# Optimization experiments

Hardware: AMD Instinct MI355X
Metric: run time of the kernel (lower is better)

Reference implementation:

```python
import jax, jax.numpy as jnp
import numpy as np

B = 1
DIM = 2048
N_HEADS = 16
HEAD_DIM = 128
RANK = 128
ALPHA = 128.0
L_NOISE = 2048
L_COND = 1024
N_LORAS = 1
EPS = 1e-6
NEG = -1e20


def setup_inputs() -> dict:
    key = jax.random.key(0)
    ks = jax.random.split(key, 24)
    inp = {}
    inp["noise_flat"] = jax.random.normal(ks[0], (B, L_NOISE, DIM), jnp.float32)
    inp["cond_flat"] = jax.random.normal(ks[1], (B, L_COND, DIM), jnp.float32)
    # RoPE freqs in TE 'bshd' convention: (L, head_dim), halves duplicated
    inv_freq = 1.0 / (10000.0 ** (jnp.arange(0, HEAD_DIM, 2, dtype=jnp.float32) / HEAD_DIM))
    pos = jnp.arange(L_NOISE + L_COND, dtype=jnp.float32)
    fr = pos[:, None] * inv_freq[None, :]
    fr = jnp.concatenate([fr, fr], axis=-1)  # (L, HEAD_DIM)
    inp["noise_rope"] = fr[:L_NOISE]
    inp["cond_rope"] = fr[L_NOISE:]
    std = 0.02
    inp["Wq"] = jax.random.normal(ks[2], (DIM, DIM), jnp.float32) * std
    inp["Wk"] = jax.random.normal(ks[3], (DIM, DIM), jnp.float32) * std
    inp["Wv"] = jax.random.normal(ks[4], (DIM, DIM), jnp.float32) * std
    inp["Wo"] = jax.random.normal(ks[5], (DIM, DIM), jnp.float32) * std
    inp["bq"] = jnp.zeros((DIM,), jnp.float32)
    inp["bk"] = jnp.zeros((DIM,), jnp.float32)
    inp["bv"] = jnp.zeros((DIM,), jnp.float32)
    inp["bo"] = jnp.zeros((DIM,), jnp.float32)
    inp["q_norm_scale"] = jnp.ones((HEAD_DIM,), jnp.float32)
    inp["k_norm_scale"] = jnp.ones((HEAD_DIM,), jnp.float32)
    inp["v_norm_scale"] = jnp.ones((HEAD_DIM,), jnp.float32)
    # LoRA: down ~ N(0, 1/rank); up small nonzero (torch inits zeros, made nonzero for a meaningful baseline)
    for name, ki in zip(["q", "k", "v", "o"], range(6, 10)):
        k1, k2 = jax.random.split(ks[ki])
        inp[f"lora_{name}_down"] = jax.random.normal(k1, (DIM, RANK), jnp.float32) / RANK
        inp[f"lora_{name}_up"] = jax.random.normal(k2, (RANK, DIM), jnp.float32) * 0.01
    return inp


def _rms_norm(x, scale):
    return x * jax.lax.rsqrt(jnp.mean(x * x, axis=-1, keepdims=True) + EPS) * scale


def _rotate_half(x):
    x1, x2 = jnp.split(x, 2, axis=-1)
    return jnp.concatenate([-x2, x1], axis=-1)


def _apply_rope(x, freqs):
    # x: (B, L, H, D), freqs: (L, D)
    cos = jnp.cos(freqs)[None, :, None, :]
    sin = jnp.sin(freqs)[None, :, None, :]
    return x * cos + _rotate_half(x) * sin


def _block_mask():
    # noise rows attend to everything; cond block i attends only to itself
    L = L_NOISE + L_COND * N_LORAS
    idx = jnp.arange(L)
    is_noise = idx < L_NOISE
    blk = (idx - L_NOISE) // L_COND
    allowed = is_noise[:, None] | (
        (~is_noise[:, None]) & (~is_noise[None, :]) & (blk[:, None] == blk[None, :])
    )
    return jnp.where(allowed, 0.0, NEG).astype(jnp.float32)  # (L, L)


def _cond_mask(i, L):
    idx = jnp.arange(L)
    start = L_NOISE + i * L_COND
    return ((idx >= start) & (idx < start + L_COND)).astype(jnp.float32)[None, :, None]


def reference(noise_flat, cond_flat, noise_rope, cond_rope,
              Wq, Wk, Wv, Wo, bq, bk, bv, bo,
              q_norm_scale, k_norm_scale, v_norm_scale,
              lora_q_down, lora_q_up, lora_k_down, lora_k_up,
              lora_v_down, lora_v_up, lora_o_down, lora_o_up):
    joint = jnp.concatenate([noise_flat, cond_flat], axis=1)  # (B, L, D)
    rope = jnp.concatenate([noise_rope, cond_rope], axis=0)   # (L, HEAD_DIM)
    L = joint.shape[1]
    scale_lora = ALPHA / RANK
    m = _cond_mask(0, L)  # n_loras = 1, lora_weight = 1.0
    jm = joint * m

    def lora(x_masked, Wd, Wu):
        return (x_masked @ Wd) @ Wu * scale_lora

    q = joint @ Wq + bq + lora(jm, lora_q_down, lora_q_up)
    k = joint @ Wk + bk + lora(jm, lora_k_down, lora_k_up)
    v = joint @ Wv + bv + lora(jm, lora_v_down, lora_v_up)

    q = q.reshape(B, L, N_HEADS, HEAD_DIM)
    k = k.reshape(B, L, N_HEADS, HEAD_DIM)
    v = v.reshape(B, L, N_HEADS, HEAD_DIM)
    q = _rms_norm(q, q_norm_scale)
    k = _rms_norm(k, k_norm_scale)
    v = _rms_norm(v, v_norm_scale)
    q = _apply_rope(q, rope)
    k = _apply_rope(k, rope)

    bias = _block_mask()[None, None]  # (1,1,L,L)
    scores = jnp.einsum('bqhd,bkhd->bhqk', q, k) / jnp.sqrt(jnp.float32(HEAD_DIM)) + bias
    attn = jax.nn.softmax(scores, axis=-1)
    x = jnp.einsum('bhqk,bkhd->bqhd', attn, v).reshape(B, L, DIM)

    out = x @ Wo + bo + lora(x * m, lora_o_down, lora_o_up)
    return out[:, :L_NOISE, :], out[:, L_NOISE:, :]
```

## Files before the change

kernel.cpp:

```cpp
#include <hip/hip_runtime.h>

typedef _Float16 f16;
typedef _Float16 half8 __attribute__((ext_vector_type(8)));
typedef float floatx4 __attribute__((ext_vector_type(4)));

#define L_TOT   3072
#define L_NZ    2048
#define DIM_C   2048
#define NH      16
#define HD      128

__device__ __forceinline__ void gl_lds16(const f16* g, f16* l) {
    __builtin_amdgcn_global_load_lds((__attribute__((address_space(1))) void*)g,
                                     (__attribute__((address_space(3))) void*)l,
                                     16, 0, 0);
}

__global__ void sentinel_kernel(float* out) { out[0] = 1.0e6f; }

__global__ __launch_bounds__(256)
void cast_f32_f16(const float* __restrict__ in, f16* __restrict__ out, int n) {
    int i = (blockIdx.x * 256 + threadIdx.x) * 4;
    if (i + 3 < n) {
        float4 v = *(const float4*)(in + i);
        out[i+0] = (f16)v.x; out[i+1] = (f16)v.y;
        out[i+2] = (f16)v.z; out[i+3] = (f16)v.w;
    }
}

template<typename TIN>
__global__ __launch_bounds__(256)
void transpose_cast(const TIN* __restrict__ in, f16* __restrict__ out,
                    int R, int C, long long inBatch, long long outBatch) {
    in  += (long long)blockIdx.z * inBatch;
    out += (long long)blockIdx.z * outBatch;
    __shared__ f16 tile[32][33];
    int x = threadIdx.x & 31, y0 = threadIdx.x >> 5;
    int r0 = blockIdx.y * 32, c0 = blockIdx.x * 32;
#pragma unroll
    for (int i = 0; i < 4; ++i) {
        int y = y0 + i * 8;
        tile[y][x] = (f16)(float)in[(size_t)(r0 + y) * C + (c0 + x)];
    }
    __syncthreads();
#pragma unroll
    for (int i = 0; i < 4; ++i) {
        int y = y0 + i * 8;
        out[(size_t)(c0 + y) * R + (r0 + x)] = tile[x][y];
    }
}

template<int WRITE_HALF, int ACCUM, int ADD_BIAS, int SPLIT3>
__global__ __launch_bounds__(256, 2)
void gemm_tn(const f16* __restrict__ A, const f16* __restrict__ BT,
             void* __restrict__ Cv,
             const float* __restrict__ bias0, const float* __restrict__ bias1,
             const float* __restrict__ bias2,
             int M, int N, int K, int lda, int ldb, int ldc, float cscale) {
    __shared__ __align__(16) f16 lds[2][2][128 * 64];
    const int tid  = threadIdx.x;
    const int lane = tid & 63, wave = tid >> 6;
    const int m0 = blockIdx.y * 128, n0 = blockIdx.x * 128;
    const int wr = wave >> 1, wc = wave & 1;
    floatx4 acc[4][4] = {};

    const int r0i = tid >> 3;
    const int gch = (tid & 7) ^ (r0i & 7);
    const f16* gA0 = A  + (size_t)(m0 + r0i) * lda + gch * 8;
    const f16* gB0 = BT + (size_t)(n0 + r0i) * ldb + gch * 8;
    const int ldsW = wave * 512;

    auto stage = [&](int buf, int k0) {
#pragma unroll
        for (int is = 0; is < 4; ++is)
            gl_lds16(gA0 + k0 + (size_t)is * 32 * lda, &lds[buf][0][0] + is * 2048 + ldsW);
#pragma unroll
        for (int is = 0; is < 4; ++is)
            gl_lds16(gB0 + k0 + (size_t)is * 32 * ldb, &lds[buf][1][0] + is * 2048 + ldsW);
    };

    const int rl = lane & 15, cq = lane >> 4;

    const int nIter = K >> 6;
    stage(0, 0);
    int cur = 0;
    for (int t = 0; t < nIter; ++t) {
        const int k0n = (t + 1 < nIter) ? (t + 1) * 64 : 0;
        stage(cur ^ 1, k0n);
        asm volatile("s_waitcnt vmcnt(8)" ::: "memory");
        __builtin_amdgcn_s_barrier();
        __builtin_amdgcn_sched_barrier(0);

#pragma unroll
        for (int kh = 0; kh < 2; ++kh) {
            half8 af[4], bf[4];
#pragma unroll
            for (int m = 0; m < 4; ++m) {
                int row = wr * 64 + m * 16 + rl;
                int pos = (kh * 4 + cq) ^ (row & 7);
                af[m] = *(const half8*)(&lds[cur][0][row * 64 + pos * 8]);
            }
#pragma unroll
            for (int n = 0; n < 4; ++n) {
                int row = wc * 64 + n * 16 + rl;
                int pos = (kh * 4 + cq) ^ (row & 7);
                bf[n] = *(const half8*)(&lds[cur][1][row * 64 + pos * 8]);
            }
#pragma unroll
            for (int m = 0; m < 4; ++m)
#pragma unroll
                for (int n = 0; n < 4; ++n)
                    acc[m][n] = __builtin_amdgcn_mfma_f32_16x16x32_f16(af[m], bf[n], acc[m][n], 0, 0, 0);
        }
        __builtin_amdgcn_s_barrier();
        __builtin_amdgcn_sched_barrier(0);
        cur ^= 1;
    }

    const int rq = lane >> 4;
    const float* bias = bias0;
    size_t cbase = 0;
    if (SPLIT3) {
        int chunk = n0 >> 11;
        bias = (chunk == 0) ? bias0 : ((chunk == 1) ? bias1 : bias2);
        cbase = (size_t)chunk * ((size_t)L_TOT * DIM_C);
    }
#pragma unroll
    for (int m = 0; m < 4; ++m) {
        int row = m0 + wr * 64 + m * 16 + rq * 4;
#pragma unroll
        for (int n = 0; n < 4; ++n) {
            int col = n0 + wc * 64 + n * 16 + rl;
            float badd = ADD_BIAS ? bias[SPLIT3 ? (col & 2047) : col] : 0.0f;
            int ccol = SPLIT3 ? (col & 2047) : col;
#pragma unroll
            for (int j = 0; j < 4; ++j) {
                float v = acc[m][n][j] * cscale + badd;
                size_t idx = cbase + (size_t)(row + j) * ldc + ccol;
                if (WRITE_HALF) {
                    f16* C = (f16*)Cv;
                    if (ACCUM) v += (float)C[idx];
                    C[idx] = (f16)v;
                } else {
                    float* C = (float*)Cv;
                    if (ACCUM) v += C[idx];
                    C[idx] = v;
                }
            }
        }
    }
}

__global__ __launch_bounds__(128)
void norm_rope_kernel(const f16* __restrict__ q16, const f16* __restrict__ k16, const f16* __restrict__ v16,
                      const float* __restrict__ qs, const float* __restrict__ ks, const float* __restrict__ vs,
                      const float* __restrict__ nrope, const float* __restrict__ crope,
                      f16* __restrict__ qH, f16* __restrict__ kH, f16* __restrict__ vH) {
    const int r = blockIdx.x, h = blockIdx.y, d = threadIdx.x;
    const size_t src = (size_t)r * DIM_C + h * HD + d;
    float qv = (float)q16[src], kv = (float)k16[src], vv = (float)v16[src];
    float sq = qv * qv, sk = kv * kv, sv = vv * vv;
#pragma unroll
    for (int m = 1; m < 64; m <<= 1) {
        sq += __shfl_xor(sq, m);
        sk += __shfl_xor(sk, m);
        sv += __shfl_xor(sv, m);
    }
    __shared__ float part[3][2];
    const int wid = d >> 6;
    if ((d & 63) == 0) { part[0][wid] = sq; part[1][wid] = sk; part[2][wid] = sv; }
    __syncthreads();
    float rq = rsqrtf((part[0][0] + part[0][1]) * (1.0f / 128.0f) + 1e-6f);
    float rk = rsqrtf((part[1][0] + part[1][1]) * (1.0f / 128.0f) + 1e-6f);
    float rv = rsqrtf((part[2][0] + part[2][1]) * (1.0f / 128.0f) + 1e-6f);
    float qn = qv * rq * qs[d];
    float kn = kv * rk * ks[d];
    float vn = vv * rv * vs[d];
    __shared__ float shq[128], shk[128];
    shq[d] = qn; shk[d] = kn;
    __syncthreads();
    float rotq = (d < 64) ? -shq[d + 64] : shq[d - 64];
    float rotk = (d < 64) ? -shk[d + 64] : shk[d - 64];
    const float* rp = (r < L_NZ) ? (nrope + (size_t)r * HD) : (crope + (size_t)(r - L_NZ) * HD);
    float fr = rp[d];
    float c = cosf(fr), s = sinf(fr);
    const size_t dst = ((size_t)h * L_TOT + r) * HD + d;
    qH[dst] = (f16)((qn * c + rotq * s) * 0.08838834764831845f);
    kH[dst] = (f16)(kn * c + rotk * s);
    vH[dst] = (f16)vn;
}

__global__ __launch_bounds__(256, 2)
void flash_kernel(const f16* __restrict__ qH, const f16* __restrict__ kH,
                  const f16* __restrict__ vT, f16* __restrict__ xH) {
    __shared__ __align__(16) f16 lds_k[2][64 * 128];
    __shared__ __align__(16) f16 lds_v[64 * 128];
    __shared__ __align__(16) f16 p_lds[4][32][72];
    const int tid = threadIdx.x;
    const int lane = tid & 63, w = tid >> 6;
    const int bid = blockIdx.x;
    const int xcd = bid & 7, rr = bid >> 3;
    int h, qb;
    if (rr < 16) { h = xcd + 8 * (rr >> 3); qb = 16 + (rr & 7); }
    else         { int li = rr - 16; h = xcd + 8 * (li >> 4); qb = li & 15; }
    const int q0 = qb * 128 + w * 32;
    const int rl = lane & 15, rq = lane >> 4;

    half8 aq[2][4];
    const f16* qbase = qH + ((size_t)h * L_TOT + q0) * HD;
#pragma unroll
    for (int qt = 0; qt < 2; ++qt)
#pragma unroll
        for (int kc = 0; kc < 4; ++kc)
            aq[qt][kc] = *(const half8*)(qbase + (size_t)(qt * 16 + rl) * HD + kc * 32 + rq * 8);

    floatx4 acc[2][8] = {};
    floatx4 accl[2] = {};
    const half8 vone = {(f16)1.f, (f16)1.f, (f16)1.f, (f16)1.f,
                        (f16)1.f, (f16)1.f, (f16)1.f, (f16)1.f};

    const int kLo = (qb >= 16) ? L_NZ : 0;
    const f16* khead = kH + (size_t)h * L_TOT * HD;
    const f16* vhead = vT + (size_t)h * HD * L_TOT;

    auto stageK = [&](int kb, int pb) {
#pragma unroll
        for (int is = 0; is < 4; ++is) {
            int i = is * 256 + tid;
            int r = i >> 4, c = i & 15;
            gl_lds16(khead + (size_t)(kb + r) * HD + ((c ^ (r & 15)) * 8),
                     &lds_k[pb][0] + (is * 256 + w * 64) * 8);
        }
    };
    auto stageV = [&](int kb) {
#pragma unroll
        for (int is = 0; is < 4; ++is) {
            int i = is * 256 + tid;
            int pair = i >> 4, c10 = i & 15;
            int g10 = c10 ^ (pair & 15);
            int d = pair * 2 + (g10 >> 3), kchunk = g10 & 7;
            gl_lds16(vhead + (size_t)d * L_TOT + kb + kchunk * 8,
                     lds_v + (is * 256 + w * 64) * 8);
        }
    };

    asm volatile("s_waitcnt vmcnt(0)" ::: "memory");
    stageK(kLo, 0);
    int p = 0;
    for (int kb = kLo; kb < L_TOT; kb += 64) {
        const int kbn = (kb + 64 < L_TOT) ? (kb + 64) : kLo;
        stageV(kb);
        stageK(kbn, p ^ 1);
        asm volatile("s_waitcnt vmcnt(8)" ::: "memory");
        __builtin_amdgcn_s_barrier();
        __builtin_amdgcn_sched_barrier(0);

        const f16* kbase = &lds_k[p][0];
        floatx4 sacc[2][4] = {};
#pragma unroll
        for (int kf = 0; kf < 4; ++kf) {
            int r = kf * 16 + rl;
#pragma unroll
            for (int kc = 0; kc < 4; ++kc) {
                half8 bk = *(const half8*)(kbase + r * 128 + (((kc * 4 + rq) ^ (r & 15)) * 8));
                sacc[0][kf] = __builtin_amdgcn_mfma_f32_16x16x32_f16(aq[0][kc], bk, sacc[0][kf], 0, 0, 0);
                sacc[1][kf] = __builtin_amdgcn_mfma_f32_16x16x32_f16(aq[1][kc], bk, sacc[1][kf], 0, 0, 0);
            }
        }
#pragma unroll
        for (int qt = 0; qt < 2; ++qt)
#pragma unroll
            for (int kf = 0; kf < 4; ++kf)
#pragma unroll
                for (int j = 0; j < 4; ++j) {
                    float pv = __expf(sacc[qt][kf][j] - 4.0f);
                    p_lds[w][qt * 16 + rq * 4 + j][kf * 16 + rl] = (f16)pv;
                }

        asm volatile("s_waitcnt vmcnt(4)" ::: "memory");
        __builtin_amdgcn_s_barrier();
        __builtin_amdgcn_sched_barrier(0);

#pragma unroll
        for (int kc = 0; kc < 2; ++kc) {
            half8 ap0 = *(const half8*)(&p_lds[w][0 * 16 + rl][kc * 32 + rq * 8]);
            half8 ap1 = *(const half8*)(&p_lds[w][1 * 16 + rl][kc * 32 + rq * 8]);
            accl[0] = __builtin_amdgcn_mfma_f32_16x16x32_f16(ap0, vone, accl[0], 0, 0, 0);
            accl[1] = __builtin_amdgcn_mfma_f32_16x16x32_f16(ap1, vone, accl[1], 0, 0, 0);
#pragma unroll
            for (int dt = 0; dt < 8; ++dt) {
                int d = dt * 16 + rl;
                int g10 = (d & 1) * 8 + kc * 4 + rq;
                half8 bv = *(const half8*)(lds_v + (d >> 1) * 128 + ((g10 ^ ((d >> 1) & 15)) * 8));
                acc[0][dt] = __builtin_amdgcn_mfma_f32_16x16x32_f16(ap0, bv, acc[0][dt], 0, 0, 0);
                acc[1][dt] = __builtin_amdgcn_mfma_f32_16x16x32_f16(ap1, bv, acc[1][dt], 0, 0, 0);
            }
        }
        __builtin_amdgcn_s_barrier();
        p ^= 1;
    }

#pragma unroll
    for (int qt = 0; qt < 2; ++qt)
#pragma unroll
        for (int j = 0; j < 4; ++j) {
            float li = 1.0f / accl[qt][j];
            int row = q0 + qt * 16 + rq * 4 + j;
#pragma unroll
            for (int dt = 0; dt < 8; ++dt)
                xH[(size_t)row * DIM_C + h * HD + dt * 16 + rl] = (f16)(acc[qt][dt][j] * li);
        }
}

extern "C" void kernel_launch(void* const* d_in, const int* in_sizes, int n_in,
                              void* d_out, int out_size, void* d_ws, size_t ws_size,
                              hipStream_t stream) {
    const float* noise = (const float*)d_in[0];
    const float* cond  = (const float*)d_in[1];
    const float* nrope = (const float*)d_in[2];
    const float* crope = (const float*)d_in[3];
    const float* Wq = (const float*)d_in[4];
    const float* Wk = (const float*)d_in[5];
    const float* Wv = (const float*)d_in[6];
    const float* Wo = (const float*)d_in[7];
    const float* bq = (const float*)d_in[8];
    const float* bk = (const float*)d_in[9];
    const float* bv = (const float*)d_in[10];
    const float* bo = (const float*)d_in[11];
    const float* qs = (const float*)d_in[12];
    const float* ks = (const float*)d_in[13];
    const float* vs = (const float*)d_in[14];
    const float* lqd = (const float*)d_in[15];
    const float* lqu = (const float*)d_in[16];
    const float* lkd = (const float*)d_in[17];
    const float* lku = (const float*)d_in[18];
    const float* lvd = (const float*)d_in[19];
    const float* lvu = (const float*)d_in[20];
    const float* lod = (const float*)d_in[21];
    const float* lou = (const float*)d_in[22];
    (void)in_sizes; (void)n_in; (void)out_size;

    char* ws = (char*)d_ws;
    const size_t SZ_LD = (size_t)L_TOT * DIM_C * sizeof(f16);
    const size_t SZ_W  = (size_t)DIM_C * DIM_C * sizeof(f16);
    size_t o = 0;
    auto take = [&](size_t b) { size_t r = o; o += (b + 255) & ~(size_t)255; return r; };
    f16* jointH   = (f16*)(ws + take(SZ_LD));
    f16* WTqkv    = (f16*)(ws + take(3 * SZ_W));
    f16* WT3      = (f16*)(ws + take(SZ_W));
    f16* downTqkv = (f16*)(ws + take((size_t)384 * 2048 * 2));
    f16* downTo   = (f16*)(ws + take((size_t)128 * 2048 * 2));
    f16* upT0     = (f16*)(ws + take((size_t)2048 * 128 * 2));
    f16* upT1     = (f16*)(ws + take((size_t)2048 * 128 * 2));
    f16* upT2     = (f16*)(ws + take((size_t)2048 * 128 * 2));
    f16* upTo     = (f16*)(ws + take((size_t)2048 * 128 * 2));
    f16* q16      = (f16*)(ws + take(3 * SZ_LD));
    f16* k16      = q16 + (size_t)L_TOT * DIM_C;
    f16* v16      = k16 + (size_t)L_TOT * DIM_C;
    f16* t_all    = (f16*)(ws + take((size_t)1024 * 384 * 2));
    f16* t_o      = (f16*)(ws + take((size_t)1024 * 128 * 2));
    f16* qHd      = (f16*)(ws + take(SZ_LD));
    f16* kHd      = (f16*)(ws + take(SZ_LD));
    f16* vHd      = (f16*)(ws + take(SZ_LD));
    f16* vTd      = (f16*)(ws + take(SZ_LD));
    f16* xH       = (f16*)(ws + take(SZ_LD));
    if (o > ws_size) {
        sentinel_kernel<<<1, 1, 0, stream>>>((float*)d_out);
        return;
    }

    cast_f32_f16<<<dim3((2048 * 2048) / 1024), 256, 0, stream>>>(noise, jointH, 2048 * 2048);
    cast_f32_f16<<<dim3((1024 * 2048) / 1024), 256, 0, stream>>>(cond, jointH + (size_t)2048 * 2048, 1024 * 2048);
    transpose_cast<float><<<dim3(64, 64, 1), 256, 0, stream>>>(Wq, WTqkv,                          2048, 2048, 0, 0);
    transpose_cast<float><<<dim3(64, 64, 1), 256, 0, stream>>>(Wk, WTqkv + (size_t)2048 * 2048,     2048, 2048, 0, 0);
    transpose_cast<float><<<dim3(64, 64, 1), 256, 0, stream>>>(Wv, WTqkv + (size_t)2 * 2048 * 2048, 2048, 2048, 0, 0);
    transpose_cast<float><<<dim3(64, 64, 1), 256, 0, stream>>>(Wo, WT3, 2048, 2048, 0, 0);
    transpose_cast<float><<<dim3(4, 64, 1), 256, 0, stream>>>(lqd, downTqkv,                      2048, 128, 0, 0);
    transpose_cast<float><<<dim3(4, 64, 1), 256, 0, stream>>>(lkd, downTqkv + (size_t)128 * 2048, 2048, 128, 0, 0);
    transpose_cast<float><<<dim3(4, 64, 1), 256, 0, stream>>>(lvd, downTqkv + (size_t)256 * 2048, 2048, 128, 0, 0);
    transpose_cast<float><<<dim3(4, 64, 1), 256, 0, stream>>>(lod, downTo, 2048, 128, 0, 0);
    transpose_cast<float><<<dim3(64, 4, 1), 256, 0, stream>>>(lqu, upT0, 128, 2048, 0, 0);
    transpose_cast<float><<<dim3(64, 4, 1), 256, 0, stream>>>(lku, upT1, 128, 2048, 0, 0);
    transpose_cast<float><<<dim3(64, 4, 1), 256, 0, stream>>>(lvu, upT2, 128, 2048, 0, 0);
    transpose_cast<float><<<dim3(64, 4, 1), 256, 0, stream>>>(lou, upTo, 128, 2048, 0, 0);

    gemm_tn<1, 0, 1, 1><<<dim3(6144 / 128, 3072 / 128), 256, 0, stream>>>(
        jointH, WTqkv, q16, bq, bk, bv, 3072, 6144, 2048, 2048, 2048, 2048, 1.0f);
    gemm_tn<1, 0, 0, 0><<<dim3(3, 8), 256, 0, stream>>>(jointH + (size_t)2048 * 2048, downTqkv, t_all,
                                                        nullptr, nullptr, nullptr,
                                                        1024, 384, 2048, 2048, 2048, 384, 1.0f);
    dim3 gup(2048 / 128, 1024 / 128);
    gemm_tn<1, 1, 0, 0><<<gup, 256, 0, stream>>>(t_all + 0,   upT0, q16 + (size_t)2048 * 2048,
                                                 nullptr, nullptr, nullptr, 1024, 2048, 128, 384, 128, 2048, 1.0f);
    gemm_tn<1, 1, 0, 0><<<gup, 256, 0, stream>>>(t_all + 128, upT1, k16 + (size_t)2048 * 2048,
                                                 nullptr, nullptr, nullptr, 1024, 2048, 128, 384, 128, 2048, 1.0f);
    gemm_tn<1, 1, 0, 0><<<gup, 256, 0, stream>>>(t_all + 256, upT2, v16 + (size_t)2048 * 2048,
                                                 nullptr, nullptr, nullptr, 1024, 2048, 128, 384, 128, 2048, 1.0f);

    norm_rope_kernel<<<dim3(3072, 16), 128, 0, stream>>>(q16, k16, v16, qs, ks, vs, nrope, crope, qHd, kHd, vHd);
    transpose_cast<f16><<<dim3(4, 96, 16), 256, 0, stream>>>(vHd, vTd, 3072, 128,
                                                             (long long)3072 * 128, (long long)128 * 3072);

    flash_kernel<<<dim3(384), 256, 0, stream>>>(qHd, kHd, vTd, xH);

    gemm_tn<0, 0, 1, 0><<<dim3(16, 24), 256, 0, stream>>>(xH, WT3, d_out, bo, nullptr, nullptr,
                                                          3072, 2048, 2048, 2048, 2048, 2048, 1.0f);
    gemm_tn<1, 0, 0, 0><<<dim3(1, 8), 256, 0, stream>>>(xH + (size_t)2048 * 2048, downTo, t_o,
                                                        nullptr, nullptr, nullptr,
                                                        1024, 128, 2048, 2048, 2048, 128, 1.0f);
    gemm_tn<0, 1, 0, 0><<<gup, 256, 0, stream>>>(t_o, upTo, (float*)d_out + (size_t)2048 * 2048,
                                                 nullptr, nullptr, nullptr,
                                                 1024, 2048, 128, 128, 128, 2048, 1.0f);
}
```

Measured before the change: 402.6 us.

## Batch preprocessing launches, merge LoRA-up GEMMs, fuse V transpose into norm-rope

Merges the two input casts into one launch, the twelve weight transposes into three z-batched launches, and the three LoRA up-projection GEMMs into a single launch whose A pointer is offset per output chunk. The norm/RoPE kernel is rewritten to process 32 rows per block with vectorized half8 loads and stores, and it writes V already transposed through an LDS tile, removing a separate transpose kernel and an intermediate buffer. The flash kernel also raises wave priority around its MFMA sections. Together these cut launch count and memory traffic, at the cost of a more complex norm kernel with heavier register use.

After: 355.6 us. -11.7%, faster.

```diff
diff --git a/kernel.cpp b/kernel.cpp
--- a/kernel.cpp
+++ b/kernel.cpp
@@ -19,28 +19,30 @@
 __global__ void sentinel_kernel(float* out) { out[0] = 1.0e6f; }
 
 __global__ __launch_bounds__(256)
-void cast_f32_f16(const float* __restrict__ in, f16* __restrict__ out, int n) {
+void cast_joint(const float* __restrict__ noise, const float* __restrict__ cond,
+                f16* __restrict__ out) {
     int i = (blockIdx.x * 256 + threadIdx.x) * 4;
-    if (i + 3 < n) {
-        float4 v = *(const float4*)(in + i);
-        out[i+0] = (f16)v.x; out[i+1] = (f16)v.y;
-        out[i+2] = (f16)v.z; out[i+3] = (f16)v.w;
-    }
-}
-
-template<typename TIN>
+    const float* src; int off;
+    if (i < 2048 * 2048) { src = noise; off = i; }
+    else                 { src = cond;  off = i - 2048 * 2048; }
+    float4 v = *(const float4*)(src + off);
+    out[i+0] = (f16)v.x; out[i+1] = (f16)v.y;
+    out[i+2] = (f16)v.z; out[i+3] = (f16)v.w;
+}
+
 __global__ __launch_bounds__(256)
-void transpose_cast(const TIN* __restrict__ in, f16* __restrict__ out,
-                    int R, int C, long long inBatch, long long outBatch) {
-    in  += (long long)blockIdx.z * inBatch;
-    out += (long long)blockIdx.z * outBatch;
+void transpose_cast4(const float* __restrict__ s0, const float* __restrict__ s1,
+                     const float* __restrict__ s2, const float* __restrict__ s3,
+                     f16* __restrict__ dstBase, int R, int C, long long outBatch) {
+    const float* in = (blockIdx.z == 0) ? s0 : (blockIdx.z == 1) ? s1 : (blockIdx.z == 2) ? s2 : s3;
+    f16* out = dstBase + (long long)blockIdx.z * outBatch;
     __shared__ f16 tile[32][33];
     int x = threadIdx.x & 31, y0 = threadIdx.x >> 5;
     int r0 = blockIdx.y * 32, c0 = blockIdx.x * 32;
 #pragma unroll
     for (int i = 0; i < 4; ++i) {
         int y = y0 + i * 8;
-        tile[y][x] = (f16)(float)in[(size_t)(r0 + y) * C + (c0 + x)];
+        tile[y][x] = (f16)in[(size_t)(r0 + y) * C + (c0 + x)];
     }
     __syncthreads();
 #pragma unroll
@@ -50,7 +52,7 @@
     }
 }
 
-template<int WRITE_HALF, int ACCUM, int ADD_BIAS, int SPLIT3>
+template<int WRITE_HALF, int ACCUM, int ADD_BIAS, int MODE>
 __global__ __launch_bounds__(256, 2)
 void gemm_tn(const f16* __restrict__ A, const f16* __restrict__ BT,
              void* __restrict__ Cv,
@@ -64,6 +66,8 @@
     const int wr = wave >> 1, wc = wave & 1;
     floatx4 acc[4][4] = {};
 
+    if (MODE == 2) A += (size_t)(n0 >> 11) * 128;
+
     const int r0i = tid >> 3;
     const int gch = (tid & 7) ^ (r0i & 7);
     const f16* gA0 = A  + (size_t)(m0 + r0i) * lda + gch * 8;
@@ -120,9 +124,9 @@
     const int rq = lane >> 4;
     const float* bias = bias0;
     size_t cbase = 0;
-    if (SPLIT3) {
+    if (MODE == 1 || MODE == 2) {
         int chunk = n0 >> 11;
-        bias = (chunk == 0) ? bias0 : ((chunk == 1) ? bias1 : bias2);
+        if (MODE == 1) bias = (chunk == 0) ? bias0 : ((chunk == 1) ? bias1 : bias2);
         cbase = (size_t)chunk * ((size_t)L_TOT * DIM_C);
     }
 #pragma unroll
@@ -131,8 +135,8 @@
 #pragma unroll
         for (int n = 0; n < 4; ++n) {
             int col = n0 + wc * 64 + n * 16 + rl;
-            float badd = ADD_BIAS ? bias[SPLIT3 ? (col & 2047) : col] : 0.0f;
-            int ccol = SPLIT3 ? (col & 2047) : col;
+            int ccol = (MODE == 1 || MODE == 2) ? (col & 2047) : col;
+            float badd = ADD_BIAS ? bias[ccol] : 0.0f;
 #pragma unroll
             for (int j = 0; j < 4; ++j) {
                 float v = acc[m][n][j] * cscale + badd;
@@ -151,43 +155,65 @@
     }
 }
 
-__global__ __launch_bounds__(128)
-void norm_rope_kernel(const f16* __restrict__ q16, const f16* __restrict__ k16, const f16* __restrict__ v16,
-                      const float* __restrict__ qs, const float* __restrict__ ks, const float* __restrict__ vs,
-                      const float* __restrict__ nrope, const float* __restrict__ crope,
-                      f16* __restrict__ qH, f16* __restrict__ kH, f16* __restrict__ vH) {
-    const int r = blockIdx.x, h = blockIdx.y, d = threadIdx.x;
-    const size_t src = (size_t)r * DIM_C + h * HD + d;
-    float qv = (float)q16[src], kv = (float)k16[src], vv = (float)v16[src];
-    float sq = qv * qv, sk = kv * kv, sv = vv * vv;
-#pragma unroll
-    for (int m = 1; m < 64; m <<= 1) {
-        sq += __shfl_xor(sq, m);
-        sk += __shfl_xor(sk, m);
-        sv += __shfl_xor(sv, m);
-    }
-    __shared__ float part[3][2];
-    const int wid = d >> 6;
-    if ((d & 63) == 0) { part[0][wid] = sq; part[1][wid] = sk; part[2][wid] = sv; }
+__global__ __launch_bounds__(256)
+void norm_rope_v(const f16* __restrict__ q16, const f16* __restrict__ k16, const f16* __restrict__ v16,
+                 const float* __restrict__ qs, const float* __restrict__ ks, const float* __restrict__ vs,
+                 const float* __restrict__ nrope, const float* __restrict__ crope,
+                 f16* __restrict__ qH, f16* __restrict__ kH, f16* __restrict__ vT) {
+    __shared__ f16 vtile[128][33];
+    const int t = threadIdx.x, rloc = t >> 3, c = t & 7;
+    const int r = blockIdx.x * 32 + rloc, h = blockIdx.y;
+    const int d0 = c * 8;
+    const size_t src = (size_t)r * DIM_C + h * HD;
+    half8 qlv = *(const half8*)(q16 + src + d0);
+    half8 qhv = *(const half8*)(q16 + src + 64 + d0);
+    half8 klv = *(const half8*)(k16 + src + d0);
+    half8 khv = *(const half8*)(k16 + src + 64 + d0);
+    half8 vlv = *(const half8*)(v16 + src + d0);
+    half8 vhv = *(const half8*)(v16 + src + 64 + d0);
+    float ql[8], qh[8], kl[8], kh[8], vl[8], vh[8];
+    float sq = 0.f, sk = 0.f, sv = 0.f;
+#pragma unroll
+    for (int i = 0; i < 8; ++i) {
+        ql[i] = (float)qlv[i]; qh[i] = (float)qhv[i];
+        kl[i] = (float)klv[i]; kh[i] = (float)khv[i];
+        vl[i] = (float)vlv[i]; vh[i] = (float)vhv[i];
+        sq += ql[i]*ql[i] + qh[i]*qh[i];
+        sk += kl[i]*kl[i] + kh[i]*kh[i];
+        sv += vl[i]*vl[i] + vh[i]*vh[i];
+    }
+    sq += __shfl_xor(sq, 1); sq += __shfl_xor(sq, 2); sq += __shfl_xor(sq, 4);
+    sk += __shfl_xor(sk, 1); sk += __shfl_xor(sk, 2); sk += __shfl_xor(sk, 4);
+    sv += __shfl_xor(sv, 1); sv += __shfl_xor(sv, 2); sv += __shfl_xor(sv, 4);
+    const float rqs = rsqrtf(sq * (1.0f / 128.0f) + 1e-6f);
+    const float rks = rsqrtf(sk * (1.0f / 128.0f) + 1e-6f);
+    const float rvs = rsqrtf(sv * (1.0f / 128.0f) + 1e-6f);
+    const float* rp = (r < L_NZ) ? (nrope + (size_t)r * HD) : (crope + (size_t)(r - L_NZ) * HD);
+    half8 qo_l, qo_h, ko_l, ko_h;
+#pragma unroll
+    for (int i = 0; i < 8; ++i) {
+        float fr = rp[d0 + i];
+        float cs = cosf(fr), sn = sinf(fr);
+        float qnl = ql[i] * rqs * qs[d0 + i],      qnh = qh[i] * rqs * qs[64 + d0 + i];
+        float knl = kl[i] * rks * ks[d0 + i],      knh = kh[i] * rks * ks[64 + d0 + i];
+        qo_l[i] = (f16)((qnl * cs - qnh * sn) * 0.08838834764831845f);
+        qo_h[i] = (f16)((qnh * cs + qnl * sn) * 0.08838834764831845f);
+        ko_l[i] = (f16)(knl * cs - knh * sn);
+        ko_h[i] = (f16)(knh * cs + knl * sn);
+        vtile[d0 + i][rloc]      = (f16)(vl[i] * rvs * vs[d0 + i]);
+        vtile[64 + d0 + i][rloc] = (f16)(vh[i] * rvs * vs[64 + d0 + i]);
+    }
+    const size_t dst = ((size_t)h * L_TOT + r) * HD;
+    *(half8*)(qH + dst + d0) = qo_l;      *(half8*)(qH + dst + 64 + d0) = qo_h;
+    *(half8*)(kH + dst + d0) = ko_l;      *(half8*)(kH + dst + 64 + d0) = ko_h;
     __syncthreads();
-    float rq = rsqrtf((part[0][0] + part[0][1]) * (1.0f / 128.0f) + 1e-6f);
-    float rk = rsqrtf((part[1][0] + part[1][1]) * (1.0f / 128.0f) + 1e-6f);
-    float rv = rsqrtf((part[2][0] + part[2][1]) * (1.0f / 128.0f) + 1e-6f);
-    float qn = qv * rq * qs[d];
-    float kn = kv * rk * ks[d];
-    float vn = vv * rv * vs[d];
-    __shared__ float shq[128], shk[128];
-    shq[d] = qn; shk[d] = kn;
-    __syncthreads();
-    float rotq = (d < 64) ? -shq[d + 64] : shq[d - 64];
-    float rotk = (d < 64) ? -shk[d + 64] : shk[d - 64];
-    const float* rp = (r < L_NZ) ? (nrope + (size_t)r * HD) : (crope + (size_t)(r - L_NZ) * HD);
-    float fr = rp[d];
-    float c = cosf(fr), s = sinf(fr);
-    const size_t dst = ((size_t)h * L_TOT + r) * HD + d;
-    qH[dst] = (f16)((qn * c + rotq * s) * 0.08838834764831845f);
-    kH[dst] = (f16)(kn * c + rotk * s);
-    vH[dst] = (f16)vn;
+    const int dd = t >> 1, seg = (t & 1) * 16;
+    half8 o0, o1;
+#pragma unroll
+    for (int i = 0; i < 8; ++i) { o0[i] = vtile[dd][seg + i]; o1[i] = vtile[dd][seg + 8 + i]; }
+    f16* vdst = vT + ((size_t)h * HD + dd) * L_TOT + blockIdx.x * 32 + seg;
+    *(half8*)(vdst)     = o0;
+    *(half8*)(vdst + 8) = o1;
 }
 
 __global__ __launch_bounds__(256, 2)
@@ -257,6 +283,7 @@
 
         const f16* kbase = &lds_k[p][0];
         floatx4 sacc[2][4] = {};
+        __builtin_amdgcn_s_setprio(1);
 #pragma unroll
         for (int kf = 0; kf < 4; ++kf) {
             int r = kf * 16 + rl;
@@ -267,6 +294,7 @@
                 sacc[1][kf] = __builtin_amdgcn_mfma_f32_16x16x32_f16(aq[1][kc], bk, sacc[1][kf], 0, 0, 0);
             }
         }
+        __builtin_amdgcn_s_setprio(0);
 #pragma unroll
         for (int qt = 0; qt < 2; ++qt)
 #pragma unroll
@@ -281,6 +309,7 @@
         __builtin_amdgcn_s_barrier();
         __builtin_amdgcn_sched_barrier(0);
 
+        __builtin_amdgcn_s_setprio(1);
 #pragma unroll
         for (int kc = 0; kc < 2; ++kc) {
             half8 ap0 = *(const half8*)(&p_lds[w][0 * 16 + rl][kc * 32 + rq * 8]);
@@ -296,6 +325,7 @@
                 acc[1][dt] = __builtin_amdgcn_mfma_f32_16x16x32_f16(ap1, bv, acc[1][dt], 0, 0, 0);
             }
         }
+        __builtin_amdgcn_s_setprio(0);
         __builtin_amdgcn_s_barrier();
         p ^= 1;
     }
@@ -345,61 +375,46 @@
     const size_t SZ_W  = (size_t)DIM_C * DIM_C * sizeof(f16);
     size_t o = 0;
     auto take = [&](size_t b) { size_t r = o; o += (b + 255) & ~(size_t)255; return r; };
-    f16* jointH   = (f16*)(ws + take(SZ_LD));
-    f16* WTqkv    = (f16*)(ws + take(3 * SZ_W));
-    f16* WT3      = (f16*)(ws + take(SZ_W));
-    f16* downTqkv = (f16*)(ws + take((size_t)384 * 2048 * 2));
-    f16* downTo   = (f16*)(ws + take((size_t)128 * 2048 * 2));
-    f16* upT0     = (f16*)(ws + take((size_t)2048 * 128 * 2));
-    f16* upT1     = (f16*)(ws + take((size_t)2048 * 128 * 2));
-    f16* upT2     = (f16*)(ws + take((size_t)2048 * 128 * 2));
-    f16* upTo     = (f16*)(ws + take((size_t)2048 * 128 * 2));
-    f16* q16      = (f16*)(ws + take(3 * SZ_LD));
-    f16* k16      = q16 + (size_t)L_TOT * DIM_C;
-    f16* v16      = k16 + (size_t)L_TOT * DIM_C;
-    f16* t_all    = (f16*)(ws + take((size_t)1024 * 384 * 2));
-    f16* t_o      = (f16*)(ws + take((size_t)1024 * 128 * 2));
-    f16* qHd      = (f16*)(ws + take(SZ_LD));
-    f16* kHd      = (f16*)(ws + take(SZ_LD));
-    f16* vHd      = (f16*)(ws + take(SZ_LD));
-    f16* vTd      = (f16*)(ws + take(SZ_LD));
-    f16* xH       = (f16*)(ws + take(SZ_LD));
+    f16* jointH = (f16*)(ws + take(SZ_LD));
+    f16* WTqkv  = (f16*)(ws + take(4 * SZ_W));
+    f16* WT3    = WTqkv + (size_t)3 * 2048 * 2048;
+    f16* downT  = (f16*)(ws + take((size_t)4 * 128 * 2048 * 2));
+    f16* downTo = downT + (size_t)3 * 128 * 2048;
+    f16* upT    = (f16*)(ws + take((size_t)4 * 2048 * 128 * 2));
+    f16* upTo   = upT + (size_t)3 * 2048 * 128;
+    f16* q16    = (f16*)(ws + take(3 * SZ_LD));
+    f16* k16    = q16 + (size_t)L_TOT * DIM_C;
+    f16* v16    = k16 + (size_t)L_TOT * DIM_C;
+    f16* t_all  = (f16*)(ws + take((size_t)1024 * 384 * 2));
+    f16* t_o    = (f16*)(ws + take((size_t)1024 * 128 * 2));
+    f16* qHd    = (f16*)(ws + take(SZ_LD));
+    f16* kHd    = (f16*)(ws + take(SZ_LD));
+    f16* vTd    = (f16*)(ws + take(SZ_LD));
+    f16* xH     = (f16*)(ws + take(SZ_LD));
     if (o > ws_size) {
         sentinel_kernel<<<1, 1, 0, stream>>>((float*)d_out);
         return;
     }
 
-    cast_f32_f16<<<dim3((2048 * 2048) / 1024), 256, 0, stream>>>(noise, jointH, 2048 * 2048);
-    cast_f32_f16<<<dim3((1024 * 2048) / 1024), 256, 0, stream>>>(cond, jointH + (size_t)2048 * 2048, 1024 * 2048);
-    transpose_cast<float><<<dim3(64, 64, 1), 256, 0, stream>>>(Wq, WTqkv,                          2048, 2048, 0, 0);
-    transpose_cast<float><<<dim3(64, 64, 1), 256, 0, stream>>>(Wk, WTqkv + (size_t)2048 * 2048,     2048, 2048, 0, 0);
-    transpose_cast<float><<<dim3(64, 64, 1), 256, 0, stream>>>(Wv, WTqkv + (size_t)2 * 2048 * 2048, 2048, 2048, 0, 0);
-    transpose_cast<float><<<dim3(64, 64, 1), 256, 0, stream>>>(Wo, WT3, 2048, 2048, 0, 0);
-    transpose_cast<float><<<dim3(4, 64, 1), 256, 0, stream>>>(lqd, downTqkv,                      2048, 128, 0, 0);
-    transpose_cast<float><<<dim3(4, 64, 1), 256, 0, stream>>>(lkd, downTqkv + (size_t)128 * 2048, 2048, 128, 0, 0);
-    transpose_cast<float><<<dim3(4, 64, 1), 256, 0, stream>>>(lvd, downTqkv + (size_t)256 * 2048, 2048, 128, 0, 0);
-    transpose_cast<float><<<dim3(4, 64, 1), 256, 0, stream>>>(lod, downTo, 2048, 128, 0, 0);
-    transpose_cast<float><<<dim3(64, 4, 1), 256, 0, stream>>>(lqu, upT0, 128, 2048, 0, 0);
-    transpose_cast<float><<<dim3(64, 4, 1), 256, 0, stream>>>(lku, upT1, 128, 2048, 0, 0);
-    transpose_cast<float><<<dim3(64, 4, 1), 256, 0, stream>>>(lvu, upT2, 128, 2048, 0, 0);
-    transpose_cast<float><<<dim3(64, 4, 1), 256, 0, stream>>>(lou, upTo, 128, 2048, 0, 0);
-
-    gemm_tn<1, 0, 1, 1><<<dim3(6144 / 128, 3072 / 128), 256, 0, stream>>>(
+    cast_joint<<<dim3(6144), 256, 0, stream>>>(noise, cond, jointH);
+    transpose_cast4<<<dim3(64, 64, 4), 256, 0, stream>>>(Wq, Wk, Wv, Wo, WTqkv, 2048, 2048,
+                                                         (long long)2048 * 2048);
+    transpose_cast4<<<dim3(4, 64, 4), 256, 0, stream>>>(lqd, lkd, lvd, lod, downT, 2048, 128,
+                                                        (long long)128 * 2048);
+    transpose_cast4<<<dim3(64, 4, 4), 256, 0, stream>>>(lqu, lku, lvu, lou, upT, 128, 2048,
+                                                        (long long)2048 * 128);
+
+    gemm_tn<1, 0, 1, 1><<<dim3(48, 24), 256, 0, stream>>>(
         jointH, WTqkv, q16, bq, bk, bv, 3072, 6144, 2048, 2048, 2048, 2048, 1.0f);
-    gemm_tn<1, 0, 0, 0><<<dim3(3, 8), 256, 0, stream>>>(jointH + (size_t)2048 * 2048, downTqkv, t_all,
+    gemm_tn<1, 0, 0, 0><<<dim3(3, 8), 256, 0, stream>>>(jointH + (size_t)2048 * 2048, downT, t_all,
                                                         nullptr, nullptr, nullptr,
                                                         1024, 384, 2048, 2048, 2048, 384, 1.0f);
-    dim3 gup(2048 / 128, 1024 / 128);
-    gemm_tn<1, 1, 0, 0><<<gup, 256, 0, stream>>>(t_all + 0,   upT0, q16 + (size_t)2048 * 2048,
-                                                 nullptr, nullptr, nullptr, 1024, 2048, 128, 384, 128, 2048, 1.0f);
-    gemm_tn<1, 1, 0, 0><<<gup, 256, 0, stream>>>(t_all + 128, upT1, k16 + (size_t)2048 * 2048,
-                                                 nullptr, nullptr, nullptr, 1024, 2048, 128, 384, 128, 2048, 1.0f);
-    gemm_tn<1, 1, 0, 0><<<gup, 256, 0, stream>>>(t_all + 256, upT2, v16 + (size_t)2048 * 2048,
-                                                 nullptr, nullptr, nullptr, 1024, 2048, 128, 384, 128, 2048, 1.0f);
-
-    norm_rope_kernel<<<dim3(3072, 16), 128, 0, stream>>>(q16, k16, v16, qs, ks, vs, nrope, crope, qHd, kHd, vHd);
-    transpose_cast<f16><<<dim3(4, 96, 16), 256, 0, stream>>>(vHd, vTd, 3072, 128,
-                                                             (long long)3072 * 128, (long long)128 * 3072);
+    gemm_tn<1, 1, 0, 2><<<dim3(48, 8), 256, 0, stream>>>(t_all, upT, q16 + (size_t)2048 * 2048,
+                                                         nullptr, nullptr, nullptr,
+                                                         1024, 6144, 128, 384, 128, 2048, 1.0f);
+
+    norm_rope_v<<<dim3(96, 16), 256, 0, stream>>>(q16, k16, v16, qs, ks, vs, nrope, crope,
+                                                  qHd, kHd, vTd);
 
     flash_kernel<<<dim3(384), 256, 0, stream>>>(qHd, kHd, vTd, xH);
 
@@ -408,7 +423,7 @@
     gemm_tn<1, 0, 0, 0><<<dim3(1, 8), 256, 0, stream>>>(xH + (size_t)2048 * 2048, downTo, t_o,
                                                         nullptr, nullptr, nullptr,
                                                         1024, 128, 2048, 2048, 2048, 128, 1.0f);
-    gemm_tn<0, 1, 0, 0><<<gup, 256, 0, stream>>>(t_o, upTo, (float*)d_out + (size_t)2048 * 2048,
-                                                 nullptr, nullptr, nullptr,
-                                                 1024, 2048, 128, 128, 128, 2048, 1.0f);
-}
+    gemm_tn<0, 1, 0, 0><<<dim3(16, 8), 256, 0, stream>>>(t_o, upTo, (float*)d_out + (size_t)2048 * 2048,
+                                                         nullptr, nullptr, nullptr,
+                                                         1024, 2048, 128, 128, 128, 2048, 1.0f);
+}
```
